# Kernel tuning notes

Hardware: AMD Instinct MI355X
Metric: run time of the kernel (lower is better)

Reference implementation:

```python
import jax, jax.numpy as jnp
import numpy as np

N_NODES = 100000
N_EDGES = 1600000
D_IN = 128
D_OUT = 128
ALPHA = 0.01   # LeakyReLU negative slope
BN_EPS = 1e-5


def setup_inputs() -> dict:
    key = jax.random.key(0)
    ks = jax.random.split(key, 4)
    x = jax.random.normal(ks[0], (N_NODES, D_IN), dtype=jnp.float32)
    edge_idx = jax.random.randint(ks[1], (2, N_EDGES), 0, N_NODES, dtype=jnp.int64)
    # SAGEConv params: lin_l (neighbor path, with bias) and lin_r (root path, no bias)
    s = 1.0 / np.sqrt(D_IN)
    W_l = jax.random.uniform(ks[2], (D_OUT, D_IN), jnp.float32, -s, s)
    b_l = jnp.zeros((D_OUT,), jnp.float32)
    W_r = jax.random.uniform(ks[3], (D_OUT, D_IN), jnp.float32, -s, s)
    gamma = jnp.ones((D_OUT,), jnp.float32)
    beta = jnp.zeros((D_OUT,), jnp.float32)
    return {"x": x, "edge_idx": edge_idx, "W_l": W_l, "b_l": b_l,
            "W_r": W_r, "gamma": gamma, "beta": beta}


def reference(x, edge_idx, W_l, b_l, W_r, gamma, beta):
    src = edge_idx[0]
    dst = edge_idx[1]
    # mean aggregation of source-node features at target nodes (PyG SAGEConv default)
    msg_sum = jax.ops.segment_sum(x[src], dst, num_segments=N_NODES)      # [N, D_IN]
    cnt = jax.ops.segment_sum(jnp.ones((src.shape[0],), x.dtype), dst,
                              num_segments=N_NODES)                        # [N]
    mean = msg_sum / jnp.maximum(cnt, 1.0)[:, None]
    # out = lin_l(mean_agg) + lin_r(x)
    h = mean @ W_l.T + b_l + x @ W_r.T                                     # [N, D_OUT]
    # BatchNorm1d in training mode (biased variance over node dim)
    mu = jnp.mean(h, axis=0)
    var = jnp.mean((h - mu) ** 2, axis=0)
    h = gamma * (h - mu) * jax.lax.rsqrt(var + BN_EPS) + beta
    # LeakyReLU
    return jnp.where(h >= 0, h, ALPHA * h)
```

## Files before the change

kernel.cpp:

```cpp
#include <hip/hip_runtime.h>
#include <hip/hip_bf16.h>
#include <stdint.h>

#define N_NODES 100000
#define N_EDGES 1600000
#define DIM     128
#define ALPHA   0.01f
#define BN_EPS  1e-5f
#define NBUCK   3125
#define NBLK_P  128
#define EPB     12500
#define SRT_CAP 1536
#define GEMM_GRID 391

typedef __bf16 bf16x8 __attribute__((ext_vector_type(8)));
typedef float  f32x4  __attribute__((ext_vector_type(4)));
typedef float  f32x2  __attribute__((ext_vector_type(2)));

#if defined(__has_builtin)
#if __has_builtin(__builtin_amdgcn_cvt_pk_fp8_f32) && __has_builtin(__builtin_amdgcn_cvt_pk_f32_fp8)
#define USE_FP8_BUILTIN 1
#endif
#endif

static const size_t OFF_SUM   = 512;
static const size_t OFF_SUMSQ = 1024;
static const size_t OFF_BBASE = 2048;
static const size_t OFF_BT    = 14592;
static const size_t OFF_TMP   = 32768;
static const size_t OFF_BFRAG = 6432768;
static const size_t OFF_AMEAN = 6498304;
static const size_t OFF_X8    = 32098304;
static const size_t OFF_H     = 44898304;
static const size_t OFF_XB    = 70498304;
static const size_t OFF_GHIST = 96098304;
static const size_t OFF_SOFFT = 97698304;

__device__ __forceinline__ float bf2f(unsigned short h) {
    return __uint_as_float(((unsigned int)h) << 16);
}
__device__ __forceinline__ float bflo(unsigned int w) {
    return __uint_as_float(w << 16);
}
__device__ __forceinline__ float bfhi(unsigned int w) {
    return __uint_as_float(w & 0xffff0000u);
}
__device__ __forceinline__ unsigned short f2bf(float f) {
    unsigned int u = __float_as_uint(f);
    u = u + 0x7fffu + ((u >> 16) & 1u);
    return (unsigned short)(u >> 16);
}
__device__ __forceinline__ unsigned int pack2(float a, float b) {
    return (unsigned int)f2bf(a) | ((unsigned int)f2bf(b) << 16);
}
__device__ __forceinline__ float loadS(const void* p, int i, int isf32) {
    return isf32 ? ((const float*)p)[i] : bf2f(((const unsigned short*)p)[i]);
}
__device__ __forceinline__ int edge_at(const void* e, long long i, int idx64) {
    return idx64 ? (int)((const long long*)e)[i] : ((const int*)e)[i];
}
__device__ __forceinline__ int blkpos(int k) { return ((k & 7) << 4) | (k >> 3); }

__device__ __forceinline__ void gload_lds16(const void* g, void* l) {
    __builtin_amdgcn_global_load_lds(
        reinterpret_cast<const __attribute__((address_space(1))) unsigned int*>(
            reinterpret_cast<uintptr_t>(g)),
        reinterpret_cast<__attribute__((address_space(3))) unsigned int*>(
            reinterpret_cast<uintptr_t>(l)),
        16, 0, 0);
}

#ifndef USE_FP8_BUILTIN
__device__ __forceinline__ unsigned int enc_fp8_1(float f) {
    unsigned int u = __float_as_uint(f);
    unsigned int s = (u >> 24) & 0x80u;
    unsigned int au = u & 0x7fffffffu;
    if (au >= 0x43E00000u) return s | 0x7Eu;
    if (au < 0x3C800000u) {
        int m = (int)rintf(__uint_as_float(au) * 512.0f);
        return s | (unsigned int)m;
    }
    unsigned int r = au + 0x7FFFFu + ((au >> 20) & 1u);
    unsigned int e = (r >> 23) & 0xffu;
    unsigned int m3 = (r >> 20) & 7u;
    return s | ((e - 120u) << 3) | m3;
}
#endif
__device__ __forceinline__ unsigned int enc4(float f0, float f1, float f2, float f3) {
#ifdef USE_FP8_BUILTIN
    int r = __builtin_amdgcn_cvt_pk_fp8_f32(f0, f1, 0, false);
    r = __builtin_amdgcn_cvt_pk_fp8_f32(f2, f3, r, true);
    return (unsigned int)r;
#else
    return enc_fp8_1(f0) | (enc_fp8_1(f1) << 8) | (enc_fp8_1(f2) << 16) | (enc_fp8_1(f3) << 24);
#endif
}
__device__ __forceinline__ void dec4(unsigned int w, float* o) {
#ifdef USE_FP8_BUILTIN
    f32x2 a = __builtin_amdgcn_cvt_pk_f32_fp8(w, false);
    f32x2 b = __builtin_amdgcn_cvt_pk_f32_fp8(w, true);
    o[0] = a[0]; o[1] = a[1]; o[2] = b[0]; o[3] = b[1];
#else
    #pragma unroll
    for (int j = 0; j < 4; j++) {
        unsigned int c = (w >> (8 * j)) & 0xffu;
        o[j] = __uint_as_float(((c & 0x80u) << 24) | ((c & 0x7fu) << 20)) * 0x1p120f;
    }
#endif
}

__device__ __forceinline__ int detect_idx64(const void* e) {
    const unsigned int* ew = (const unsigned int*)e;
    unsigned long long m = __ballot(ew[2 * (threadIdx.x & 63) + 1] != 0u);
    return (__popcll(m) < 8) ? 1 : 0;
}
__device__ __forceinline__ int detect_isf32(const void* x) {
    const unsigned int* xw = (const unsigned int*)x;
    unsigned int w = xw[threadIdx.x & 63];
    unsigned int e = (w >> 7) & 0xffu;
    bool bflike = (e >= 110u && e <= 140u) || ((w & 0xffffu) == 0u);
    unsigned long long m = __ballot(bflike);
    return (__popcll(m) > 32) ? 0 : 1;
}

__global__ __launch_bounds__(256) void k1_kernel(const void* edges, const void* x,
                                                 int* ghist, unsigned int* x8,
                                                 unsigned short* xb, float* gz) {
    int tid = threadIdx.x;
    if (blockIdx.x < NBLK_P) {
        __shared__ int sh[NBUCK];
        int idx64 = detect_idx64(edges);
        int blk = blockIdx.x;
        if (blk == 0) gz[tid] = 0.f;
        for (int i = tid; i < NBUCK; i += 256) sh[i] = 0;
        __syncthreads();
        long long base = (long long)blk * EPB;
        for (int i = tid; i < EPB; i += 256) {
            int d = edge_at(edges, (long long)N_EDGES + base + i, idx64);
            atomicAdd(&sh[d >> 5], 1);
        }
        __syncthreads();
        for (int i = tid; i < NBUCK; i += 256) ghist[blk * NBUCK + i] = sh[i];
    } else {
        int isf32 = detect_isf32(x);
        int gid = (blockIdx.x - NBLK_P) * 256 + tid;
        float f[16];
        if (!isf32) {
            const uint4* xv = (const uint4*)x;
            uint4 a = xv[gid * 2], b2 = xv[gid * 2 + 1];
            unsigned int w[8] = {a.x, a.y, a.z, a.w, b2.x, b2.y, b2.z, b2.w};
            #pragma unroll
            for (int i = 0; i < 8; i++) { f[2 * i] = bflo(w[i]); f[2 * i + 1] = bfhi(w[i]); }
        } else {
            const float4* xf = (const float4*)x;
            #pragma unroll
            for (int i = 0; i < 4; i++) {
                float4 v = xf[gid * 4 + i];
                f[4 * i] = v.x; f[4 * i + 1] = v.y; f[4 * i + 2] = v.z; f[4 * i + 3] = v.w;
            }
            uint4 h1, h2;
            h1.x = pack2(f[0], f[1]);  h1.y = pack2(f[2], f[3]);
            h1.z = pack2(f[4], f[5]);  h1.w = pack2(f[6], f[7]);
            h2.x = pack2(f[8], f[9]);  h2.y = pack2(f[10], f[11]);
            h2.z = pack2(f[12], f[13]); h2.w = pack2(f[14], f[15]);
            ((uint4*)xb)[gid * 2]     = h1;
            ((uint4*)xb)[gid * 2 + 1] = h2;
        }
        uint4 o;
        o.x = enc4(f[0], f[1], f[2], f[3]);
        o.y = enc4(f[4], f[5], f[6], f[7]);
        o.z = enc4(f[8], f[9], f[10], f[11]);
        o.w = enc4(f[12], f[13], f[14], f[15]);
        *(uint4*)(x8 + gid * 4) = o;
    }
}

__global__ __launch_bounds__(256) void p2a_kernel(const int* ghist, int* sOffT, int* bT) {
    int k = blockIdx.x, wv = threadIdx.x >> 6, lane = threadIdx.x & 63;
    int k0 = ((lane & 15) << 3) | (lane >> 4);
    int k1i = (((lane + 64) & 15) << 3) | ((lane + 64) >> 4);
    for (int g = 0; g < 4; g++) {
        int b = k * 16 + wv * 4 + g;
        if (b >= NBUCK) continue;
        int v0 = ghist[k0 * NBUCK + b];
        int v1 = ghist[k1i * NBUCK + b];
        int sc0 = v0, sc1 = v1;
        #pragma unroll
        for (int off = 1; off < 64; off <<= 1) {
            int u0 = __shfl_up(sc0, off, 64);
            int u1 = __shfl_up(sc1, off, 64);
            if (lane >= off) { sc0 += u0; sc1 += u1; }
        }
        int t0 = __shfl(sc0, 63, 64);
        sOffT[b * NBLK_P + lane] = sc0 - v0;
        sOffT[b * NBLK_P + 64 + lane] = t0 + sc1 - v1;
        if (lane == 63) bT[b] = t0 + sc1;
    }
}

__global__ __launch_bounds__(256) void k3_kernel(const int* bT, int* bucketBase,
                                                 const void* W_l, const void* W_r,
                                                 const void* x, unsigned short* bfrag) {
    int t = threadIdx.x;
    if (blockIdx.x == 0) {
        __shared__ int ws[4];
        int base = t * 13;
        int v[13]; int s = 0;
        #pragma unroll
        for (int i = 0; i < 13; i++) {
            int idx = base + i;
            v[i] = (idx < NBUCK) ? bT[idx] : 0;
            s += v[i];
        }
        int lane = t & 63, wv = t >> 6;
        int sc = s;
        #pragma unroll
        for (int off = 1; off < 64; off <<= 1) {
            int u = __shfl_up(sc, off, 64);
            if (lane >= off) sc += u;
        }
        if (lane == 63) ws[wv] = sc;
        __syncthreads();
        int add = 0;
        for (int w = 0; w < wv; w++) add += ws[w];
        int run = sc - s + add;
        #pragma unroll
        for (int i = 0; i < 13; i++) {
            int idx = base + i;
            if (idx < NBUCK) bucketBase[idx] = run;
            run += v[i];
        }
    } else {
        int isf32 = detect_isf32(x);
        int g = (blockIdx.x - 1) * 256 + t;
        int j    = g & 7;
        int lane = (g >> 3) & 63;
        int s    = (g >> 9) & 7;
        int tt   = (g >> 12) & 7;
        int n = tt * 16 + (lane & 15);
        int k = s * 32 + ((lane >> 4) & 3) * 8 + j;
        float v = (k < DIM) ? loadS(W_l, n * DIM + k, isf32)
                            : loadS(W_r, n * DIM + (k - DIM), isf32);
        bfrag[g] = f2bf(v);
    }
}

__global__ __launch_bounds__(256) void p3_kernel(const void* edges, const int* sOffT,
                                                 const int* bucketBase, unsigned int* tmp) {
    __shared__ int sbase[NBUCK];
    int idx64 = detect_idx64(edges);
    int blk = blockIdx.x, tid = threadIdx.x;
    int mypos = blkpos(blk);
    for (int i = tid; i < NBUCK; i += 256)
        sbase[i] = bucketBase[i] + sOffT[i * NBLK_P + mypos];
    __syncthreads();
    long long base = (long long)blk * EPB;
    for (int i = tid; i < EPB; i += 256) {
        long long e = base + i;
        int s = edge_at(edges, e, idx64);
        int d = edge_at(edges, (long long)N_EDGES + e, idx64);
        int p = atomicAdd(&sbase[d >> 5], 1);
        tmp[p] = ((unsigned int)(d & 31) << 17) | (unsigned int)s;
    }
}

__global__ __launch_bounds__(256) void agg_kernel(const unsigned int* x8, const unsigned int* tmp,
                                                  const int* bucketBase, unsigned short* Amean) {
    __shared__ int s_cnt[32];
    __shared__ int s_beg[32];
    __shared__ int s_srt[SRT_CAP];
    int b = blockIdx.x, tid = threadIdx.x;
    int gb = bucketBase[b];
    int ge = (b == NBUCK - 1) ? N_EDGES : bucketBase[b + 1];
    int nE = min(ge - gb, SRT_CAP);
    if (tid < 32) s_cnt[tid] = 0;
    __syncthreads();
    for (int i = tid; i < nE; i += 256) atomicAdd(&s_cnt[tmp[gb + i] >> 17], 1);
    __syncthreads();
    if (tid < 32) {
        int v = s_cnt[tid];
        int sc = v;
        #pragma unroll
        for (int off = 1; off < 32; off <<= 1) {
            int u = __shfl_up(sc, off, 64);
            if (tid >= off) sc += u;
        }
        s_beg[tid] = sc - v;
        s_cnt[tid] = sc - v;
    }
    __syncthreads();
    for (int i = tid; i < nE; i += 256) {
        unsigned int w = tmp[gb + i];
        int p = atomicAdd(&s_cnt[w >> 17], 1);
        s_srt[p] = (int)(w & 0x1ffffu);
    }
    __syncthreads();
    int wv = tid >> 6, lane = tid & 63;
    int oct = lane >> 3, l8 = lane & 7;
    int nl = wv * 8 + oct;
    int nb = s_beg[nl], ne2 = s_cnt[nl];
    const uint4* xv = (const uint4*)x8;
    float acc[16];
    #pragma unroll
    for (int i = 0; i < 16; i++) acc[i] = 0.f;
    for (int jj = nb; jj < ne2; jj += 4) {
        uint4 r[4]; float mk[4];
        #pragma unroll
        for (int u = 0; u < 4; u++) {
            int e = jj + u;
            int su = s_srt[(e < ne2) ? e : nb];
            mk[u] = (e < ne2) ? 1.f : 0.f;
            r[u] = xv[(size_t)su * 8 + l8];
        }
        #pragma unroll
        for (int u = 0; u < 4; u++) {
            float f[4];
            dec4(r[u].x, f);
            acc[0] = fmaf(f[0], mk[u], acc[0]);  acc[1] = fmaf(f[1], mk[u], acc[1]);
            acc[2] = fmaf(f[2], mk[u], acc[2]);  acc[3] = fmaf(f[3], mk[u], acc[3]);
            dec4(r[u].y, f);
            acc[4] = fmaf(f[0], mk[u], acc[4]);  acc[5] = fmaf(f[1], mk[u], acc[5]);
            acc[6] = fmaf(f[2], mk[u], acc[6]);  acc[7] = fmaf(f[3], mk[u], acc[7]);
            dec4(r[u].z, f);
            acc[8] = fmaf(f[0], mk[u], acc[8]);  acc[9] = fmaf(f[1], mk[u], acc[9]);
            acc[10] = fmaf(f[2], mk[u], acc[10]); acc[11] = fmaf(f[3], mk[u], acc[11]);
            dec4(r[u].w, f);
            acc[12] = fmaf(f[0], mk[u], acc[12]); acc[13] = fmaf(f[1], mk[u], acc[13]);
            acc[14] = fmaf(f[2], mk[u], acc[14]); acc[15] = fmaf(f[3], mk[u], acc[15]);
        }
    }
    int ng = b * 32 + nl;
    float inv = 1.0f / (float)max(ne2 - nb, 1);
    uint4 o1, o2;
    o1.x = pack2(acc[0] * inv, acc[1] * inv);
    o1.y = pack2(acc[2] * inv, acc[3] * inv);
    o1.z = pack2(acc[4] * inv, acc[5] * inv);
    o1.w = pack2(acc[6] * inv, acc[7] * inv);
    o2.x = pack2(acc[8] * inv, acc[9] * inv);
    o2.y = pack2(acc[10] * inv, acc[11] * inv);
    o2.z = pack2(acc[12] * inv, acc[13] * inv);
    o2.w = pack2(acc[14] * inv, acc[15] * inv);
    *(uint4*)(Amean + (size_t)ng * 128 + l8 * 16) = o1;
    *(uint4*)(Amean + (size_t)ng * 128 + l8 * 16 + 8) = o2;
}

__global__ __launch_bounds__(256, 2) void gemm_kernel(const unsigned short* __restrict__ Amean,
                                                      const void* __restrict__ x,
                                                      const unsigned short* __restrict__ xb,
                                                      const unsigned short* __restrict__ Bfrag_g,
                                                      const void* __restrict__ b_l,
                                                      unsigned int* __restrict__ Hu,
                                                      float* __restrict__ gpart) {
    __shared__ unsigned short lds[32768];
    __shared__ float sstat[2][128];
    int isf32 = detect_isf32(x);
    const unsigned short* xs = isf32 ? xb : (const unsigned short*)x;
    int tid = threadIdx.x;
    int wave = tid >> 6, lane = tid & 63;
    int lm = lane & 15, lq = lane >> 4;

    #pragma unroll
    for (int k = 0; k < 16; k++) {
        int e = tid + k * 256;
        gload_lds16(Bfrag_g + (size_t)e * 8, lds + (size_t)e * 8);
    }
    if (tid < 128) { sstat[0][tid] = 0.f; sstat[1][tid] = 0.f; }

    int base = blockIdx.x * 256;
    bf16x8 aq[4][8];
    #pragma unroll
    for (int j = 0; j < 4; j++) {
        int rowA = base + (wave * 4 + j) * 16 + lm;
        if (rowA >= N_NODES) rowA = N_NODES - 1;
        const unsigned short* am = Amean + (size_t)rowA * 128 + lq * 8;
        const unsigned short* xm = xs + (size_t)rowA * 128 + lq * 8;
        #pragma unroll
        for (int s = 0; s < 4; s++) aq[j][s] = *(const bf16x8*)(am + s * 32);
        #pragma unroll
        for (int s = 0; s < 4; s++) aq[j][4 + s] = *(const bf16x8*)(xm + s * 32);
    }
    float bv[8];
    #pragma unroll
    for (int t = 0; t < 8; t++) bv[t] = loadS(b_l, t * 16 + lm, isf32);
    float st1[8], st2[8];
    #pragma unroll
    for (int t = 0; t < 8; t++) { st1[t] = 0.f; st2[t] = 0.f; }

    __syncthreads();

    #pragma unroll
    for (int j = 0; j < 4; j++) {
        f32x4 acc[8];
        #pragma unroll
        for (int t = 0; t < 8; t++) acc[t] = (f32x4){0.f, 0.f, 0.f, 0.f};
        #pragma unroll
        for (int s = 0; s < 8; s++) {
            #pragma unroll
            for (int t = 0; t < 8; t++) {
                bf16x8 bb = *(const bf16x8*)(lds + ((t * 8 + s) * 64 + lane) * 8);
                acc[t] = __builtin_amdgcn_mfma_f32_16x16x32_bf16(aq[j][s], bb, acc[t], 0, 0, 0);
            }
        }
        #pragma unroll
        for (int t = 0; t < 8; t++) {
            #pragma unroll
            for (int r = 0; r < 4; r++) {
                int ro = base + (wave * 4 + j) * 16 + lq * 4 + r;
                float v = acc[t][r] + bv[t];
                float p = __shfl_xor(v, 1, 64);
                bool in = (ro < N_NODES);
                if (in) { st1[t] += v; st2[t] += v * v; }
                if (in && !(lm & 1)) Hu[(size_t)ro * 64 + t * 8 + (lm >> 1)] = pack2(v, p);
            }
        }
    }
    #pragma unroll
    for (int t = 0; t < 8; t++) {
        atomicAdd(&sstat[0][t * 16 + lm], st1[t]);
        atomicAdd(&sstat[1][t * 16 + lm], st2[t]);
    }
    __syncthreads();
    gpart[(size_t)blockIdx.x * 256 + threadIdx.x] = ((const float*)sstat)[threadIdx.x];
}

__global__ __launch_bounds__(256) void redux_kernel(const float* gpart, float* gz) {
    int t = threadIdx.x;
    float a = 0.f;
    for (int b = blockIdx.x; b < GEMM_GRID; b += 8)
        a += gpart[(size_t)b * 256 + t];
    atomicAdd(&gz[t], a);
}

__global__ __launch_bounds__(256) void bn_norm_kernel(const unsigned int* __restrict__ Hu,
                                                      const void* x,
                                                      const float* gsum,
                                                      const float* gsumsq, const void* gamma,
                                                      const void* beta, void* out) {
    __shared__ float sc[128], sh[128];
    int isf32 = detect_isf32(x);
    int tid = threadIdx.x;
    if (tid < 128) {
        const float invN = 1.0f / (float)N_NODES;
        float mu = gsum[tid] * invN;
        float var = gsumsq[tid] * invN - mu * mu;
        float rstd = rsqrtf(var + BN_EPS);
        float g = loadS(gamma, tid, isf32);
        float b = loadS(beta, tid, isf32);
        sc[tid] = g * rstd;
        sh[tid] = b - mu * g * rstd;
    }
    __syncthreads();
    size_t idx = (size_t)blockIdx.x * 256 + tid;
    size_t i8 = idx * 8;
    float h[8];
    {
        uint4 u = *(const uint4*)(Hu + idx * 4);
        h[0]=bflo(u.x); h[1]=bfhi(u.x); h[2]=bflo(u.y); h[3]=bfhi(u.y);
        h[4]=bflo(u.z); h[5]=bfhi(u.z); h[6]=bflo(u.w); h[7]=bfhi(u.w);
    }
    int c0 = (int)(i8 & 127);
    float o[8];
    #pragma unroll
    for (int i = 0; i < 8; i++) {
        float v = h[i] * sc[c0 + i] + sh[c0 + i];
        o[i] = (v >= 0.f) ? v : ALPHA * v;
    }
    if (isf32) {
        *(float4*)((float*)out + i8) = make_float4(o[0], o[1], o[2], o[3]);
        *(float4*)((float*)out + i8 + 4) = make_float4(o[4], o[5], o[6], o[7]);
    } else {
        uint4 u;
        u.x = pack2(o[0], o[1]); u.y = pack2(o[2], o[3]);
        u.z = pack2(o[4], o[5]); u.w = pack2(o[6], o[7]);
        *(uint4*)((unsigned short*)out + i8) = u;
    }
}

extern "C" void kernel_launch(void* const* d_in, const int* in_sizes, int n_in,
                              void* d_out, int out_size, void* d_ws, size_t ws_size,
                              hipStream_t stream) {
    const void* x     = d_in[0];
    const void* eidx  = d_in[1];
    const void* W_l   = d_in[2];
    const void* b_l   = d_in[3];
    const void* W_r   = d_in[4];
    const void* gamma = d_in[5];
    const void* beta  = d_in[6];
    char* ws = (char*)d_ws;
    float* gsum = (float*)(ws + OFF_SUM);
    float* gsumsq = (float*)(ws + OFF_SUMSQ);
    int* bucketBase = (int*)(ws + OFF_BBASE);
    int* bT = (int*)(ws + OFF_BT);
    unsigned int* tmp = (unsigned int*)(ws + OFF_TMP);
    unsigned short* bfrag = (unsigned short*)(ws + OFF_BFRAG);
    unsigned short* Amean = (unsigned short*)(ws + OFF_AMEAN);
    unsigned int* x8 = (unsigned int*)(ws + OFF_X8);
    unsigned int* H = (unsigned int*)(ws + OFF_H);
    unsigned short* xb = (unsigned short*)(ws + OFF_XB);
    int* ghist = (int*)(ws + OFF_GHIST);
    int* sOffT = (int*)(ws + OFF_SOFFT);
    float* gpart = (float*)(ws + OFF_TMP);

    k1_kernel<<<NBLK_P + 3125, 256, 0, stream>>>(eidx, x, ghist, x8, xb, gsum);
    p2a_kernel<<<196, 256, 0, stream>>>(ghist, sOffT, bT);
    k3_kernel<<<129, 256, 0, stream>>>(bT, bucketBase, W_l, W_r, x, bfrag);
    p3_kernel<<<NBLK_P, 256, 0, stream>>>(eidx, sOffT, bucketBase, tmp);
    agg_kernel<<<NBUCK, 256, 0, stream>>>(x8, tmp, bucketBase, Amean);
    gemm_kernel<<<GEMM_GRID, 256, 0, stream>>>(Amean, x, xb, bfrag, b_l, H, gpart);
    redux_kernel<<<8, 256, 0, stream>>>(gpart, gsum);
    bn_norm_kernel<<<6250, 256, 0, stream>>>(H, x, gsum, gsumsq, gamma, beta, d_out);
}
```

Baseline: 283.3 us.

## Double edge-partition blocks and use serial per-bucket prefix with transposed offsets

Doubles the number of edge-partition blocks (256 blocks of 6250 edges) and runs p3 scatter with 1024 threads per block, so more CUs take part in the counting sort. The offset table is transposed to position-major, which makes p3's read of its column coalesced. p2a is rewritten so each thread serially scans one bucket across all partitions. Histogram and offset buffers are moved into the H region to reuse workspace. The serial scan in p2a uses few threads (49 blocks of 64), and sharing memory with H relies on H being written only after these buffers are no longer needed.

```diff
diff --git a/kernel.cpp b/kernel.cpp
--- a/kernel.cpp
+++ b/kernel.cpp
@@ -8,8 +8,8 @@
 #define ALPHA   0.01f
 #define BN_EPS  1e-5f
 #define NBUCK   3125
-#define NBLK_P  128
-#define EPB     12500
+#define NBLK_P  256
+#define EPB     6250
 #define SRT_CAP 1536
 #define GEMM_GRID 391
 
@@ -32,9 +32,9 @@
 static const size_t OFF_AMEAN = 6498304;
 static const size_t OFF_X8    = 32098304;
 static const size_t OFF_H     = 44898304;
+static const size_t OFF_GHIST = OFF_H;
+static const size_t OFF_SOFFT = OFF_H + 4194304;
 static const size_t OFF_XB    = 70498304;
-static const size_t OFF_GHIST = 96098304;
-static const size_t OFF_SOFFT = 97698304;
 
 __device__ __forceinline__ float bf2f(unsigned short h) {
     return __uint_as_float(((unsigned int)h) << 16);
@@ -59,7 +59,8 @@
 __device__ __forceinline__ int edge_at(const void* e, long long i, int idx64) {
     return idx64 ? (int)((const long long*)e)[i] : ((const int*)e)[i];
 }
-__device__ __forceinline__ int blkpos(int k) { return ((k & 7) << 4) | (k >> 3); }
+__device__ __forceinline__ int blkpos(int k) { return ((k & 7) << 5) | (k >> 3); }
+__device__ __forceinline__ int posblk(int p) { return ((p & 31) << 3) | (p >> 5); }
 
 __device__ __forceinline__ void gload_lds16(const void* g, void* l) {
     __builtin_amdgcn_global_load_lds(
@@ -175,27 +176,20 @@
     }
 }
 
-__global__ __launch_bounds__(256) void p2a_kernel(const int* ghist, int* sOffT, int* bT) {
-    int k = blockIdx.x, wv = threadIdx.x >> 6, lane = threadIdx.x & 63;
-    int k0 = ((lane & 15) << 3) | (lane >> 4);
-    int k1i = (((lane + 64) & 15) << 3) | ((lane + 64) >> 4);
-    for (int g = 0; g < 4; g++) {
-        int b = k * 16 + wv * 4 + g;
-        if (b >= NBUCK) continue;
-        int v0 = ghist[k0 * NBUCK + b];
-        int v1 = ghist[k1i * NBUCK + b];
-        int sc0 = v0, sc1 = v1;
-        #pragma unroll
-        for (int off = 1; off < 64; off <<= 1) {
-            int u0 = __shfl_up(sc0, off, 64);
-            int u1 = __shfl_up(sc1, off, 64);
-            if (lane >= off) { sc0 += u0; sc1 += u1; }
-        }
-        int t0 = __shfl(sc0, 63, 64);
-        sOffT[b * NBLK_P + lane] = sc0 - v0;
-        sOffT[b * NBLK_P + 64 + lane] = t0 + sc1 - v1;
-        if (lane == 63) bT[b] = t0 + sc1;
-    }
+__global__ __launch_bounds__(64) void p2a_kernel(const int* __restrict__ ghist,
+                                                 int* __restrict__ sOffT,
+                                                 int* __restrict__ bT) {
+    int b = blockIdx.x * 64 + threadIdx.x;
+    if (b >= NBUCK) return;
+    int run = 0;
+    #pragma unroll 8
+    for (int p = 0; p < NBLK_P; p++) {
+        int k = posblk(p);
+        int v = ghist[k * NBUCK + b];
+        sOffT[p * NBUCK + b] = run;
+        run += v;
+    }
+    bT[b] = run;
 }
 
 __global__ __launch_bounds__(256) void k3_kernel(const int* bT, int* bucketBase,
@@ -245,17 +239,18 @@
     }
 }
 
-__global__ __launch_bounds__(256) void p3_kernel(const void* edges, const int* sOffT,
-                                                 const int* bucketBase, unsigned int* tmp) {
+__global__ __launch_bounds__(1024) void p3_kernel(const void* edges, const int* __restrict__ sOffT,
+                                                  const int* __restrict__ bucketBase,
+                                                  unsigned int* __restrict__ tmp) {
     __shared__ int sbase[NBUCK];
     int idx64 = detect_idx64(edges);
     int blk = blockIdx.x, tid = threadIdx.x;
     int mypos = blkpos(blk);
-    for (int i = tid; i < NBUCK; i += 256)
-        sbase[i] = bucketBase[i] + sOffT[i * NBLK_P + mypos];
+    for (int i = tid; i < NBUCK; i += 1024)
+        sbase[i] = bucketBase[i] + sOffT[(size_t)mypos * NBUCK + i];
     __syncthreads();
     long long base = (long long)blk * EPB;
-    for (int i = tid; i < EPB; i += 256) {
+    for (int i = tid; i < EPB; i += 1024) {
         long long e = base + i;
         int s = edge_at(edges, e, idx64);
         int d = edge_at(edges, (long long)N_EDGES + e, idx64);
@@ -502,9 +497,9 @@
     float* gpart = (float*)(ws + OFF_TMP);
 
     k1_kernel<<<NBLK_P + 3125, 256, 0, stream>>>(eidx, x, ghist, x8, xb, gsum);
-    p2a_kernel<<<196, 256, 0, stream>>>(ghist, sOffT, bT);
+    p2a_kernel<<<49, 64, 0, stream>>>(ghist, sOffT, bT);
     k3_kernel<<<129, 256, 0, stream>>>(bT, bucketBase, W_l, W_r, x, bfrag);
-    p3_kernel<<<NBLK_P, 256, 0, stream>>>(eidx, sOffT, bucketBase, tmp);
+    p3_kernel<<<NBLK_P, 1024, 0, stream>>>(eidx, sOffT, bucketBase, tmp);
     agg_kernel<<<NBUCK, 256, 0, stream>>>(x8, tmp, bucketBase, Amean);
     gemm_kernel<<<GEMM_GRID, 256, 0, stream>>>(Amean, x, xb, bfrag, b_l, H, gpart);
     redux_kernel<<<8, 256, 0, stream>>>(gpart, gsum);
```

Result: faster. 254.2 us (-10.3%).
